# Kernel optimization log

Hardware: AMD Instinct MI355X
Metric: run time of the kernel (lower is better)

The kernel has to match this reference:

```python
import jax, jax.numpy as jnp
import numpy as np

N, C, SI, VI, H, R = 10000, 2, 128, 16, 4, 32
SH, VH = SI // H, VI // H  # 32, 4
EPS = 1e-8

def _vnorm(x, axis):
    # clamped L2 norm, matches _norm_no_nan
    return jnp.sqrt(jnp.clip(jnp.sum(x * x, axis=axis), EPS, None))

def _gvp_full(s, v, wh, ws_w, ws_b, wv, wsv_w, wsv_b):
    # GVP with activations=(silu, sigmoid), vector_gate=True, vi=vo
    vh = jnp.swapaxes(v, -1, -2) @ wh            # [..., 3, h]
    vn = _vnorm(vh, -2)                          # [..., h]
    so = jnp.concatenate([s, vn], -1) @ ws_w + ws_b
    vo = jnp.swapaxes(vh @ wv, -1, -2)           # [..., vo, 3]
    gate = jax.nn.sigmoid(jax.nn.sigmoid(so) @ wsv_w + wsv_b)
    return jax.nn.silu(so), vo * gate[..., None]

def setup_inputs():
    key = jax.random.key(0)
    ks = iter(jax.random.split(key, 40))
    def lin(i, o):
        return jax.random.normal(next(ks), (i, o), jnp.float32) / np.sqrt(i)
    def bias(o):
        return 0.02 * jax.random.normal(next(ks), (o,), jnp.float32)
    inp = {}
    inp['s'] = jax.random.normal(next(ks), (N, C, SI), jnp.float32)
    inp['v'] = jax.random.normal(next(ks), (N, C, VI, 3), jnp.float32)
    # weight_proj: GVP((SI,VI)->(R,0)), no activations; h_dim = max(VI,0) = VI
    inp['wp_wh'] = lin(VI, VI); inp['wp_ws_w'] = lin(VI + SI, R); inp['wp_ws_b'] = bias(R)
    # to_q/k/v: GVP((SI,VI)->(SI,VI)), silu/sigmoid, vector_gate; h_dim = VI
    for p in ('q', 'k', 'vv'):
        inp[p + '_wh'] = lin(VI, VI)
        inp[p + '_ws_w'] = lin(VI + SI, SI); inp[p + '_ws_b'] = bias(SI)
        inp[p + '_wv'] = lin(VI, VI)
        inp[p + '_wsv_w'] = lin(SI, VI); inp[p + '_wsv_b'] = bias(VI)
    # attn_gvp_long: GVP((2*SH, 2*VH) -> (1,0)), no activations; h_dim = 2*VH
    inp['attn_wh'] = lin(2 * VH, 2 * VH)
    inp['attn_ws_w'] = lin(2 * VH + 2 * SH, 1); inp['attn_ws_b'] = bias(1)
    return inp

def reference(s, v, wp_wh, wp_ws_w, wp_ws_b,
              q_wh, q_ws_w, q_ws_b, q_wv, q_wsv_w, q_wsv_b,
              k_wh, k_ws_w, k_ws_b, k_wv, k_wsv_w, k_wsv_b,
              vv_wh, vv_ws_w, vv_ws_b, vv_wv, vv_wsv_w, vv_wsv_b,
              attn_wh, attn_ws_w, attn_ws_b):
    n, c = s.shape[:2]
    # ---- Compress: softmax-pool N -> R anchors ----
    vh = jnp.swapaxes(v, -1, -2) @ wp_wh          # [N,C,3,VI]
    vn = _vnorm(vh, -2)                            # [N,C,VI]
    pw = jnp.concatenate([s, vn], -1) @ wp_ws_w + wp_ws_b  # [N,C,R]
    pw = jax.nn.softmax(pw, axis=0)                # softmax over nodes
    s_g = jnp.einsum('nca,ncs->acs', pw, s)        # [R,C,SI] (includes transpose(0,1))
    v_g = jnp.einsum('nca,ncvd->acvd', pw, v)      # [R,C,VI,3]
    # ---- q from nodes, k/v from anchors ----
    qs, qv = _gvp_full(s, v, q_wh, q_ws_w, q_ws_b, q_wv, q_wsv_w, q_wsv_b)
    ks, kv = _gvp_full(s_g, v_g, k_wh, k_ws_w, k_ws_b, k_wv, k_wsv_w, k_wsv_b)
    vs, vv_ = _gvp_full(s_g, v_g, vv_wh, vv_ws_w, vv_ws_b, vv_wv, vv_wsv_w, vv_wsv_b)
    qs = qs.reshape(n, c, H, SH); qv = qv.reshape(n, c, H, VH, 3)
    ks = ks.reshape(R, c, H, SH); kv = kv.reshape(R, c, H, VH, 3)
    vs = vs.reshape(R, c, H, SH); vv_ = vv_.reshape(R, c, H, VH, 3)
    # ---- attention GVP on cat(q, k): split weights instead of materializing concat ----
    wh_q, wh_k = attn_wh[:VH], attn_wh[VH:]        # wh @ cat(qv,kv) = qv@wh_q + kv@wh_k
    qh = jnp.swapaxes(qv, -1, -2) @ wh_q           # [N,C,H,3,2VH]
    kh = jnp.swapaxes(kv, -1, -2) @ wh_k           # [R,C,H,3,2VH]
    vn2 = _vnorm(qh[:, None] + kh[None], -2)       # [N,R,C,H,2VH]
    ws_q = attn_ws_w[:SH]; ws_k = attn_ws_w[SH:2 * SH]; ws_n = attn_ws_w[2 * SH:]
    e = (qs @ ws_q)[:, None] + (ks @ ws_k)[None] + vn2 @ ws_n + attn_ws_b  # [N,R,C,H,1]
    e = e[..., 0] / np.sqrt(SH)
    alpha = jax.nn.softmax(e, axis=1)              # softmax over anchors (dim=1)
    # ---- Broadcast: weighted sum of anchor values ----
    out_s = jnp.einsum('nrch,rchd->nchd', alpha, vs).reshape(n, c, SI)
    out_v = jnp.einsum('nrch,rchde->nchde', alpha, vv_).reshape(n, c, VI, 3)
    return out_s, out_v
```

## Files before the change

kernel.cpp:

```cpp
#include <hip/hip_runtime.h>
#include <hip/hip_bf16.h>


#define N_  10000
#define C_  2
#define SI_ 128
#define VI_ 16
#define H_  4
#define R_  32
#define SH_ 32
#define VH_ 4
#define NC_ (N_*C_)

typedef const float* __restrict__ fptr;

__device__ __forceinline__ float sigm(float x){ return 1.f/(1.f+__expf(-x)); }

#define OFF_LG  0
#define OFF_EQH 640000
#define OFF_SG  2720000
#define OFF_ST  2731264
#define OFF_TKH 2731392
#define OFF_TEK 2737536
#define OFF_TVS 2737792
#define OFF_TVV 2745984

__global__ __launch_bounds__(256) void kA(
    fptr s, fptr v,
    fptr wp_wh, fptr wp_ws_w, fptr wp_ws_b,
    fptr q_wh, fptr q_ws_w, fptr q_ws_b, fptr q_wv, fptr q_wsv_w, fptr q_wsv_b,
    fptr attn_wh, fptr attn_ws_w,
    float* __restrict__ lg, float* __restrict__ eqh)
{
  __shared__ __align__(16) float ARENA[160*20];
  __shared__ __align__(16) float VVs[16*48];
  __shared__ __align__(16) float VHQ[16*48];
  __shared__ __align__(16) float SO[16*128];
  __shared__ __align__(16) float GATE[16*16];
  __shared__ __align__(16) float QV[16*48];
  float* const XT  = ARENA;
  float* const SIG = ARENA;

  const int tid  = threadIdx.x;
  const int row0 = blockIdx.x * 16;

  for (int idx = tid; idx < 16*128; idx += 256){
    int r = idx >> 7, j = idx & 127;
    XT[j*20 + r] = s[(row0+r)*128 + j];
  }
  for (int idx = tid; idx < 16*48; idx += 256){
    int r = idx / 48, k = idx - r*48;
    VVs[r*48 + k] = v[(row0+r)*48 + k];
  }
  __syncthreads();

  for (int t = tid; t < 512; t += 256){
    int r = t >> 5, ii = t & 31, path = ii >> 4, i = ii & 15;
    fptr wh = path ? wp_wh : q_wh;
    float h0=0.f, h1=0.f, h2=0.f;
    #pragma unroll
    for (int j = 0; j < 16; j++){
      float w = wh[j*16 + i];
      h0 = fmaf(VVs[r*48 + j*3 + 0], w, h0);
      h1 = fmaf(VVs[r*48 + j*3 + 1], w, h1);
      h2 = fmaf(VVs[r*48 + j*3 + 2], w, h2);
    }
    float vn = sqrtf(fmaxf(h0*h0 + h1*h1 + h2*h2, 1e-8f));
    if (!path){
      VHQ[r*48 +  0 + i] = h0;
      VHQ[r*48 + 16 + i] = h1;
      VHQ[r*48 + 32 + i] = h2;
      XT[(128+i)*20 + r] = vn;
    } else {
      XT[(144+i)*20 + r] = vn;
    }
  }
  __syncthreads();

  const int colA = tid & 127, rgA = tid >> 7;
  float acc[8];
  {
    float bqs = q_ws_b[colA];
    #pragma unroll
    for (int k = 0; k < 8; k++) acc[k] = bqs;
    #pragma unroll 4
    for (int j = 0; j < 144; j++){
      float w = q_ws_w[j*128 + colA];
      const float* xp = &XT[j*20 + rgA*8];
      float4 x0 = *(const float4*)xp;
      float4 x1 = *(const float4*)(xp + 4);
      acc[0] = fmaf(x0.x, w, acc[0]); acc[1] = fmaf(x0.y, w, acc[1]);
      acc[2] = fmaf(x0.z, w, acc[2]); acc[3] = fmaf(x0.w, w, acc[3]);
      acc[4] = fmaf(x1.x, w, acc[4]); acc[5] = fmaf(x1.y, w, acc[5]);
      acc[6] = fmaf(x1.z, w, acc[6]); acc[7] = fmaf(x1.w, w, acc[7]);
    }
  }
  {
    const int col = tid & 31, rg = tid >> 5;
    float bp = wp_ws_b[col];
    float a0 = bp, a1 = bp;
    #pragma unroll 4
    for (int j = 0; j < 144; j++){
      int jj = (j < 128) ? j : (j + 16);
      float w = wp_ws_w[j*32 + col];
      const float* xp = &XT[jj*20 + rg*2];
      a0 = fmaf(xp[0], w, a0);
      a1 = fmaf(xp[1], w, a1);
    }
    const int n = (row0 >> 1) + rg;
    lg[(     col)*N_ + n] = a0;
    lg[(32 + col)*N_ + n] = a1;
  }
  __syncthreads();

  #pragma unroll
  for (int k = 0; k < 8; k++){
    float so = acc[k];
    float sg_ = sigm(so);
    SIG[(rgA*8 + k)*128 + colA] = sg_;
    SO [(rgA*8 + k)*128 + colA] = so * sg_;
  }
  __syncthreads();

  {
    const int r = tid >> 4, g = tid & 15;
    float ga = q_wsv_b[g];
    #pragma unroll 8
    for (int o = 0; o < 128; o += 4){
      float4 s4 = *(const float4*)&SIG[r*128 + o];
      ga = fmaf(s4.x, q_wsv_w[(o+0)*16 + g], ga);
      ga = fmaf(s4.y, q_wsv_w[(o+1)*16 + g], ga);
      ga = fmaf(s4.z, q_wsv_w[(o+2)*16 + g], ga);
      ga = fmaf(s4.w, q_wsv_w[(o+3)*16 + g], ga);
    }
    GATE[r*16 + g] = sigm(ga);
  }
  if (tid < 64){
    const int r = tid >> 2, h = tid & 3;
    float e = 0.f;
    #pragma unroll
    for (int t = 0; t < 32; t++)
      e = fmaf(SO[r*128 + h*32 + t], attn_ws_w[t], e);
    eqh[(row0 + r)*104 + h] = e;
  }
  __syncthreads();

  for (int t = tid; t < 16*48; t += 256){
    int r = t / 48, k = t - r*48, i = k / 3, d = k - i*3;
    float a = 0.f;
    #pragma unroll
    for (int j = 0; j < 16; j++)
      a = fmaf(VHQ[r*48 + d*16 + j], q_wv[j*16 + i], a);
    QV[r*48 + k] = a * GATE[r*16 + i];
  }
  __syncthreads();

  for (int t = tid; t < 16*96; t += 256){
    int r = t / 96, k = t - r*96;
    int h = k / 24, rem = k - h*24, d = rem >> 3, ee = rem & 7;
    float a = 0.f;
    #pragma unroll
    for (int i = 0; i < 4; i++)
      a = fmaf(QV[r*48 + (h*4 + i)*3 + d], attn_wh[i*8 + ee], a);
    eqh[(row0 + r)*104 + 8 + k] = a;
  }
}

__global__ __launch_bounds__(256) void kStats(const float* __restrict__ lg,
                                              float* __restrict__ st)
{
  const int q = blockIdx.x;
  const int tid = threadIdx.x;
  const float* col = lg + q*N_;
  __shared__ float red[256];

  float m = -1e30f;
  for (int n = tid; n < N_; n += 256) m = fmaxf(m, col[n]);
  red[tid] = m; __syncthreads();
  for (int s2 = 128; s2 > 0; s2 >>= 1){
    if (tid < s2) red[tid] = fmaxf(red[tid], red[tid + s2]);
    __syncthreads();
  }
  const float mx = red[0];
  __syncthreads();

  float sm = 0.f;
  for (int n = tid; n < N_; n += 256) sm += __expf(col[n] - mx);
  red[tid] = sm; __syncthreads();
  for (int s2 = 128; s2 > 0; s2 >>= 1){
    if (tid < s2) red[tid] += red[tid + s2];
    __syncthreads();
  }
  if (tid == 0){ st[q*2] = mx; st[q*2 + 1] = red[0]; }
}

#define CHUNK_ 50
__global__ __launch_bounds__(256) void kAccum(const float* __restrict__ lg,
                                              const float* __restrict__ st,
                                              fptr s, fptr v,
                                              float* __restrict__ sg)
{
  const int b = blockIdx.x, c = b & 1, chunk = b >> 1;
  const int n0 = chunk * CHUNK_;
  const int tid = threadIdx.x;
  const int ag = tid >> 5, dl = tid & 31;

  float mx[4], dn[4];
  #pragma unroll
  for (int aa = 0; aa < 4; aa++){
    int a = ag*4 + aa;
    mx[aa] = st[(c*32 + a)*2];
    dn[aa] = 1.f / st[(c*32 + a)*2 + 1];
  }
  float acc[4][6] = {};
  for (int n = n0; n < n0 + CHUNK_; n++){
    const int rc = n*2 + c;
    float pw[4];
    #pragma unroll
    for (int aa = 0; aa < 4; aa++)
      pw[aa] = __expf(lg[(c*32 + ag*4 + aa)*N_ + n] - mx[aa]) * dn[aa];
    #pragma unroll
    for (int dd = 0; dd < 6; dd++){
      int d = dl + 32*dd;
      if (d < 176){
        float xv = (d < 128) ? s[rc*128 + d] : v[rc*48 + d - 128];
        #pragma unroll
        for (int aa = 0; aa < 4; aa++)
          acc[aa][dd] = fmaf(pw[aa], xv, acc[aa][dd]);
      }
    }
  }
  #pragma unroll
  for (int aa = 0; aa < 4; aa++)
    #pragma unroll
    for (int dd = 0; dd < 6; dd++){
      int d = dl + 32*dd;
      if (d < 176)
        atomicAdd(&sg[(c*32 + ag*4 + aa)*176 + d], acc[aa][dd]);
    }
}

__global__ __launch_bounds__(256) void kSmall(
    const float* __restrict__ sg,
    fptr k_wh, fptr k_ws_w, fptr k_ws_b, fptr k_wv, fptr k_wsv_w, fptr k_wsv_b,
    fptr vv_wh, fptr vv_ws_w, fptr vv_ws_b, fptr vv_wv, fptr vv_wsv_w, fptr vv_wsv_b,
    fptr attn_wh, fptr attn_ws_w,
    float* __restrict__ tkh, float* __restrict__ tek,
    float* __restrict__ tvs, float* __restrict__ tvv)
{
  const int b = blockIdx.x, r = b >> 1, c = b & 1;
  const int tid = threadIdx.x;
  __shared__ float X[176];
  __shared__ float VN[2][16];
  __shared__ float VH[2][48];
  __shared__ float SOk[128], SOv[128];
  __shared__ float G[2][16];
  __shared__ float KV[48];

  if (tid < 176) X[tid] = sg[(c*32 + r)*176 + tid];
  __syncthreads();

  if (tid < 32){
    int path = tid >> 4, i = tid & 15;
    fptr wh = path ? vv_wh : k_wh;
    float h0=0.f, h1=0.f, h2=0.f;
    #pragma unroll
    for (int j = 0; j < 16; j++){
      float w = wh[j*16 + i];
      h0 = fmaf(X[128 + j*3 + 0], w, h0);
      h1 = fmaf(X[128 + j*3 + 1], w, h1);
      h2 = fmaf(X[128 + j*3 + 2], w, h2);
    }
    VH[path][ 0 + i] = h0; VH[path][16 + i] = h1; VH[path][32 + i] = h2;
    VN[path][i] = sqrtf(fmaxf(h0*h0 + h1*h1 + h2*h2, 1e-8f));
  }
  __syncthreads();

  {
    int path = tid >> 7, col = tid & 127;
    fptr W  = path ? vv_ws_w : k_ws_w;
    fptr Bb = path ? vv_ws_b : k_ws_b;
    float so = Bb[col];
    for (int j = 0; j < 128; j++) so = fmaf(X[j], W[j*128 + col], so);
    #pragma unroll
    for (int i = 0; i < 16; i++)  so = fmaf(VN[path][i], W[(128+i)*128 + col], so);
    (path ? SOv : SOk)[col] = so;
  }
  __syncthreads();

  if (tid < 32){
    int path = tid >> 4, g = tid & 15;
    fptr Wsv = path ? vv_wsv_w : k_wsv_w;
    fptr Bsv = path ? vv_wsv_b : k_wsv_b;
    const float* SOp = path ? SOv : SOk;
    float ga = Bsv[g];
    for (int o = 0; o < 128; o++)
      ga = fmaf(sigm(SOp[o]), Wsv[o*16 + g], ga);
    G[path][g] = sigm(ga);
  } else if (tid < 36){
    int h = tid - 32;
    float e = 0.f;
    #pragma unroll
    for (int t = 0; t < 32; t++){
      float so = SOk[h*32 + t];
      e = fmaf(so * sigm(so), attn_ws_w[32 + t], e);
    }
    tek[(r*2 + c)*4 + h] = e;
  } else if (tid >= 64 && tid < 192){
    int o = tid - 64;
    float so = SOv[o];
    tvs[(r*2 + c)*128 + o] = so * sigm(so);
  }
  __syncthreads();

  if (tid < 96){
    int path = tid / 48, k = tid % 48, i = k / 3, d = k - i*3;
    fptr Wv = path ? vv_wv : k_wv;
    float vo = 0.f;
    #pragma unroll
    for (int j = 0; j < 16; j++)
      vo = fmaf(VH[path][d*16 + j], Wv[j*16 + i], vo);
    float gv = vo * G[path][i];
    if (path == 0) KV[k] = gv;
    else {
      int h = i >> 2, ii = i & 3;
      tvv[(((r*2 + c)*4 + h)*4 + ii)*3 + d] = gv;
    }
  }
  __syncthreads();

  if (tid < 96){
    int h = tid / 24, rem = tid % 24, d = rem >> 3, ee = rem & 7;
    float a = 0.f;
    #pragma unroll
    for (int i = 0; i < 4; i++)
      a = fmaf(KV[(h*4 + i)*3 + d], attn_wh[(4 + i)*8 + ee], a);
    tkh[((r*2 + c)*4 + h)*24 + d*8 + ee] = a;
  }
}

__global__ __launch_bounds__(512) void kAttn(
    const float* __restrict__ eqh,
    const float* __restrict__ tkh, const float* __restrict__ tek,
    const float* __restrict__ tvs, const float* __restrict__ tvv,
    fptr attn_ws_w, fptr attn_ws_b,
    float* __restrict__ out)
{
  __shared__ __align__(16) float KH[6144];
  __shared__ __align__(16) float EK[256];
  __shared__ __align__(16) float VS[256*36];
  __shared__ __align__(16) float VVt[3072];
  const int tid = threadIdx.x;

  for (int i = tid; i < 6144; i += 512) KH[i] = tkh[i];
  if (tid < 256) EK[tid] = tek[tid];
  for (int i = tid; i < 8192; i += 512){ int base = i >> 5, t = i & 31; VS[base*36 + t] = tvs[i]; }
  for (int i = tid; i < 3072; i += 512) VVt[i] = tvv[i];

  float wsn[8];
  #pragma unroll
  for (int ee = 0; ee < 8; ee++) wsn[ee] = attn_ws_w[64 + ee];
  const float wb = attn_ws_b[0];
  __syncthreads();

  const int row = blockIdx.x*128 + (tid >> 2);
  const int h = tid & 3;
  if (row < NC_){
    const int c = row & 1;
    const float eq = eqh[row*104 + h];
    float qh[24];
    const float4* qp = (const float4*)&eqh[row*104 + 8 + h*24];
    #pragma unroll
    for (int k = 0; k < 6; k++){
      float4 t4 = qp[k];
      qh[k*4+0] = t4.x; qh[k*4+1] = t4.y; qh[k*4+2] = t4.z; qh[k*4+3] = t4.w;
    }
    float e[32];
    float em = -1e30f;
    #pragma unroll
    for (int r = 0; r < 32; r++){
      const int base = (r*2 + c)*4 + h;
      const float* khp = &KH[base*24];
      float en = 0.f;
      #pragma unroll
      for (int ee = 0; ee < 8; ee++){
        float a0 = qh[ee]      + khp[ee];
        float a1 = qh[8 + ee]  + khp[8 + ee];
        float a2 = qh[16 + ee] + khp[16 + ee];
        en = fmaf(sqrtf(fmaxf(a0*a0 + a1*a1 + a2*a2, 1e-8f)), wsn[ee], en);
      }
      float ev = (eq + EK[base] + en + wb) * 0.17677669529663687f;
      e[r] = ev; em = fmaxf(em, ev);
    }
    float den = 0.f;
    #pragma unroll
    for (int r = 0; r < 32; r++){ e[r] = __expf(e[r] - em); den += e[r]; }
    const float inv = 1.f / den;
    float accs[32] = {};
    float accv[12] = {};
    #pragma unroll
    for (int r = 0; r < 32; r++){
      const int base = (r*2 + c)*4 + h;
      const float al = e[r] * inv;
      const float* vsp = &VS[base*36];
      #pragma unroll
      for (int t = 0; t < 32; t++) accs[t] = fmaf(al, vsp[t], accs[t]);
      const float* vvp = &VVt[base*12];
      #pragma unroll
      for (int k = 0; k < 12; k++) accv[k] = fmaf(al, vvp[k], accv[k]);
    }
    float* po = &out[row*128 + h*32];
    #pragma unroll
    for (int t = 0; t < 32; t++) po[t] = accs[t];
    float* pv = &out[NC_*128 + row*48 + h*12];
    #pragma unroll
    for (int k = 0; k < 12; k++) pv[k] = accv[k];
  }
}

extern "C" void kernel_launch(void* const* d_in, const int* in_sizes, int n_in,
                              void* d_out, int out_size, void* d_ws, size_t ws_size,
                              hipStream_t stream)
{
  fptr s        = (fptr)d_in[0];
  fptr v        = (fptr)d_in[1];
  fptr wp_wh    = (fptr)d_in[2];
  fptr wp_ws_w  = (fptr)d_in[3];
  fptr wp_ws_b  = (fptr)d_in[4];
  fptr q_wh     = (fptr)d_in[5];
  fptr q_ws_w   = (fptr)d_in[6];
  fptr q_ws_b   = (fptr)d_in[7];
  fptr q_wv     = (fptr)d_in[8];
  fptr q_wsv_w  = (fptr)d_in[9];
  fptr q_wsv_b  = (fptr)d_in[10];
  fptr k_wh     = (fptr)d_in[11];
  fptr k_ws_w   = (fptr)d_in[12];
  fptr k_ws_b   = (fptr)d_in[13];
  fptr k_wv     = (fptr)d_in[14];
  fptr k_wsv_w  = (fptr)d_in[15];
  fptr k_wsv_b  = (fptr)d_in[16];
  fptr vv_wh    = (fptr)d_in[17];
  fptr vv_ws_w  = (fptr)d_in[18];
  fptr vv_ws_b  = (fptr)d_in[19];
  fptr vv_wv    = (fptr)d_in[20];
  fptr vv_wsv_w = (fptr)d_in[21];
  fptr vv_wsv_b = (fptr)d_in[22];
  fptr attn_wh  = (fptr)d_in[23];
  fptr attn_ws_w= (fptr)d_in[24];
  fptr attn_ws_b= (fptr)d_in[25];

  float* ws  = (float*)d_ws;
  float* lg  = ws + OFF_LG;
  float* eqh = ws + OFF_EQH;
  float* sg  = ws + OFF_SG;
  float* st  = ws + OFF_ST;
  float* tkh = ws + OFF_TKH;
  float* tek = ws + OFF_TEK;
  float* tvs = ws + OFF_TVS;
  float* tvv = ws + OFF_TVV;

  hipMemsetAsync(sg, 0, 11264*sizeof(float), stream);

  kA<<<NC_/16, 256, 0, stream>>>(s, v, wp_wh, wp_ws_w, wp_ws_b,
                                 q_wh, q_ws_w, q_ws_b, q_wv, q_wsv_w, q_wsv_b,
                                 attn_wh, attn_ws_w, lg, eqh);
  kStats<<<64, 256, 0, stream>>>(lg, st);
  kAccum<<<2*(N_/CHUNK_), 256, 0, stream>>>(lg, st, s, v, sg);
  kSmall<<<64, 256, 0, stream>>>(sg,
                                 k_wh, k_ws_w, k_ws_b, k_wv, k_wsv_w, k_wsv_b,
                                 vv_wh, vv_ws_w, vv_ws_b, vv_wv, vv_wsv_w, vv_wsv_b,
                                 attn_wh, attn_ws_w, tkh, tek, tvs, tvv);
  kAttn<<<(NC_ + 127)/128, 512, 0, stream>>>(eqh, tkh, tek, tvs, tvv,
                                             attn_ws_w, attn_ws_b, (float*)d_out);
}
```

Before: 253.2 us.

## Enlarge kA row tile, replace atomics with chunk partials, vectorize attention loads

```diff
diff --git a/kernel.cpp b/kernel.cpp
--- a/kernel.cpp
+++ b/kernel.cpp
@@ -16,45 +16,48 @@
 
 __device__ __forceinline__ float sigm(float x){ return 1.f/(1.f+__expf(-x)); }
 
-#define OFF_LG  0
-#define OFF_EQH 640000
-#define OFF_SG  2720000
-#define OFF_ST  2731264
-#define OFF_TKH 2731392
-#define OFF_TEK 2737536
-#define OFF_TVS 2737792
-#define OFF_TVV 2745984
-
-__global__ __launch_bounds__(256) void kA(
+#define OFF_LG   0
+#define OFF_EQH  640000
+#define OFF_ST   2731264
+#define OFF_TKH  2731392
+#define OFF_TEK  2737536
+#define OFF_TVS  2737792
+#define OFF_TVV  2745984
+#define OFF_PART 2749056
+
+#define CHUNK_  200
+#define NCHUNK_ (N_/CHUNK_)
+
+__global__ __launch_bounds__(512) void kA(
     fptr s, fptr v,
     fptr wp_wh, fptr wp_ws_w, fptr wp_ws_b,
     fptr q_wh, fptr q_ws_w, fptr q_ws_b, fptr q_wv, fptr q_wsv_w, fptr q_wsv_b,
     fptr attn_wh, fptr attn_ws_w,
     float* __restrict__ lg, float* __restrict__ eqh)
 {
-  __shared__ __align__(16) float ARENA[160*20];
-  __shared__ __align__(16) float VVs[16*48];
-  __shared__ __align__(16) float VHQ[16*48];
-  __shared__ __align__(16) float SO[16*128];
-  __shared__ __align__(16) float GATE[16*16];
-  __shared__ __align__(16) float QV[16*48];
+  __shared__ __align__(16) float ARENA[160*36];
+  __shared__ __align__(16) float VVs[32*48];
+  __shared__ __align__(16) float VHQ[32*48];
+  __shared__ __align__(16) float SO[32*128];
+  __shared__ __align__(16) float GATE[32*16];
+  __shared__ __align__(16) float QV[32*48];
   float* const XT  = ARENA;
   float* const SIG = ARENA;
 
   const int tid  = threadIdx.x;
-  const int row0 = blockIdx.x * 16;
-
-  for (int idx = tid; idx < 16*128; idx += 256){
+  const int row0 = blockIdx.x * 32;
+
+  for (int idx = tid; idx < 32*128; idx += 512){
     int r = idx >> 7, j = idx & 127;
-    XT[j*20 + r] = s[(row0+r)*128 + j];
-  }
-  for (int idx = tid; idx < 16*48; idx += 256){
+    XT[j*36 + r] = s[(row0+r)*128 + j];
+  }
+  for (int idx = tid; idx < 32*48; idx += 512){
     int r = idx / 48, k = idx - r*48;
     VVs[r*48 + k] = v[(row0+r)*48 + k];
   }
   __syncthreads();
 
-  for (int t = tid; t < 512; t += 256){
+  for (int t = tid; t < 1024; t += 512){
     int r = t >> 5, ii = t & 31, path = ii >> 4, i = ii & 15;
     fptr wh = path ? wp_wh : q_wh;
     float h0=0.f, h1=0.f, h2=0.f;
@@ -70,9 +73,9 @@
       VHQ[r*48 +  0 + i] = h0;
       VHQ[r*48 + 16 + i] = h1;
       VHQ[r*48 + 32 + i] = h2;
-      XT[(128+i)*20 + r] = vn;
+      XT[(128+i)*36 + r] = vn;
     } else {
-      XT[(144+i)*20 + r] = vn;
+      XT[(144+i)*36 + r] = vn;
     }
   }
   __syncthreads();
@@ -86,7 +89,7 @@
     #pragma unroll 4
     for (int j = 0; j < 144; j++){
       float w = q_ws_w[j*128 + colA];
-      const float* xp = &XT[j*20 + rgA*8];
+      const float* xp = &XT[j*36 + rgA*8];
       float4 x0 = *(const float4*)xp;
       float4 x1 = *(const float4*)(xp + 4);
       acc[0] = fmaf(x0.x, w, acc[0]); acc[1] = fmaf(x0.y, w, acc[1]);
@@ -103,7 +106,7 @@
     for (int j = 0; j < 144; j++){
       int jj = (j < 128) ? j : (j + 16);
       float w = wp_ws_w[j*32 + col];
-      const float* xp = &XT[jj*20 + rg*2];
+      const float* xp = &XT[jj*36 + rg*2];
       a0 = fmaf(xp[0], w, a0);
       a1 = fmaf(xp[1], w, a1);
     }
@@ -135,7 +138,7 @@
     }
     GATE[r*16 + g] = sigm(ga);
   }
-  if (tid < 64){
+  if (tid < 128){
     const int r = tid >> 2, h = tid & 3;
     float e = 0.f;
     #pragma unroll
@@ -145,7 +148,7 @@
   }
   __syncthreads();
 
-  for (int t = tid; t < 16*48; t += 256){
+  for (int t = tid; t < 32*48; t += 512){
     int r = t / 48, k = t - r*48, i = k / 3, d = k - i*3;
     float a = 0.f;
     #pragma unroll
@@ -155,7 +158,7 @@
   }
   __syncthreads();
 
-  for (int t = tid; t < 16*96; t += 256){
+  for (int t = tid; t < 32*96; t += 512){
     int r = t / 96, k = t - r*96;
     int h = k / 24, rem = k - h*24, d = rem >> 3, ee = rem & 7;
     float a = 0.f;
@@ -194,11 +197,10 @@
   if (tid == 0){ st[q*2] = mx; st[q*2 + 1] = red[0]; }
 }
 
-#define CHUNK_ 50
 __global__ __launch_bounds__(256) void kAccum(const float* __restrict__ lg,
                                               const float* __restrict__ st,
                                               fptr s, fptr v,
-                                              float* __restrict__ sg)
+                                              float* __restrict__ part)
 {
   const int b = blockIdx.x, c = b & 1, chunk = b >> 1;
   const int n0 = chunk * CHUNK_;
@@ -236,12 +238,12 @@
     for (int dd = 0; dd < 6; dd++){
       int d = dl + 32*dd;
       if (d < 176)
-        atomicAdd(&sg[(c*32 + ag*4 + aa)*176 + d], acc[aa][dd]);
+        part[(chunk*64 + c*32 + ag*4 + aa)*176 + d] = acc[aa][dd];
     }
 }
 
 __global__ __launch_bounds__(256) void kSmall(
-    const float* __restrict__ sg,
+    const float* __restrict__ part,
     fptr k_wh, fptr k_ws_w, fptr k_ws_b, fptr k_wv, fptr k_wsv_w, fptr k_wsv_b,
     fptr vv_wh, fptr vv_ws_w, fptr vv_ws_b, fptr vv_wv, fptr vv_wsv_w, fptr vv_wsv_b,
     fptr attn_wh, fptr attn_ws_w,
@@ -257,7 +259,12 @@
   __shared__ float G[2][16];
   __shared__ float KV[48];
 
-  if (tid < 176) X[tid] = sg[(c*32 + r)*176 + tid];
+  if (tid < 176){
+    float x = 0.f;
+    const float* p = part + (c*32 + r)*176 + tid;
+    for (int ch = 0; ch < NCHUNK_; ch++) x += p[(size_t)ch*64*176];
+    X[tid] = x;
+  }
   __syncthreads();
 
   if (tid < 32){
@@ -380,13 +387,19 @@
     #pragma unroll
     for (int r = 0; r < 32; r++){
       const int base = (r*2 + c)*4 + h;
-      const float* khp = &KH[base*24];
+      float khl[24];
+      const float4* kp4 = (const float4*)&KH[base*24];
+      #pragma unroll
+      for (int q = 0; q < 6; q++){
+        float4 t4 = kp4[q];
+        khl[q*4+0] = t4.x; khl[q*4+1] = t4.y; khl[q*4+2] = t4.z; khl[q*4+3] = t4.w;
+      }
       float en = 0.f;
       #pragma unroll
       for (int ee = 0; ee < 8; ee++){
-        float a0 = qh[ee]      + khp[ee];
-        float a1 = qh[8 + ee]  + khp[8 + ee];
-        float a2 = qh[16 + ee] + khp[16 + ee];
+        float a0 = qh[ee]      + khl[ee];
+        float a1 = qh[8 + ee]  + khl[8 + ee];
+        float a2 = qh[16 + ee] + khl[16 + ee];
         en = fmaf(sqrtf(fmaxf(a0*a0 + a1*a1 + a2*a2, 1e-8f)), wsn[ee], en);
       }
       float ev = (eq + EK[base] + en + wb) * 0.17677669529663687f;
@@ -402,12 +415,24 @@
     for (int r = 0; r < 32; r++){
       const int base = (r*2 + c)*4 + h;
       const float al = e[r] * inv;
-      const float* vsp = &VS[base*36];
+      const float4* vp4 = (const float4*)&VS[base*36];
       #pragma unroll
-      for (int t = 0; t < 32; t++) accs[t] = fmaf(al, vsp[t], accs[t]);
-      const float* vvp = &VVt[base*12];
+      for (int q = 0; q < 8; q++){
+        float4 t4 = vp4[q];
+        accs[q*4+0] = fmaf(al, t4.x, accs[q*4+0]);
+        accs[q*4+1] = fmaf(al, t4.y, accs[q*4+1]);
+        accs[q*4+2] = fmaf(al, t4.z, accs[q*4+2]);
+        accs[q*4+3] = fmaf(al, t4.w, accs[q*4+3]);
+      }
+      const float4* vv4 = (const float4*)&VVt[base*12];
       #pragma unroll
-      for (int k = 0; k < 12; k++) accv[k] = fmaf(al, vvp[k], accv[k]);
+      for (int q = 0; q < 3; q++){
+        float4 t4 = vv4[q];
+        accv[q*4+0] = fmaf(al, t4.x, accv[q*4+0]);
+        accv[q*4+1] = fmaf(al, t4.y, accv[q*4+1]);
+        accv[q*4+2] = fmaf(al, t4.z, accv[q*4+2]);
+        accv[q*4+3] = fmaf(al, t4.w, accv[q*4+3]);
+      }
     }
     float* po = &out[row*128 + h*32];
     #pragma unroll
@@ -449,24 +474,22 @@
   fptr attn_ws_w= (fptr)d_in[24];
   fptr attn_ws_b= (fptr)d_in[25];
 
-  float* ws  = (float*)d_ws;
-  float* lg  = ws + OFF_LG;
-  float* eqh = ws + OFF_EQH;
-  float* sg  = ws + OFF_SG;
-  float* st  = ws + OFF_ST;
-  float* tkh = ws + OFF_TKH;
-  float* tek = ws + OFF_TEK;
-  float* tvs = ws + OFF_TVS;
-  float* tvv = ws + OFF_TVV;
-
-  hipMemsetAsync(sg, 0, 11264*sizeof(float), stream);
-
-  kA<<<NC_/16, 256, 0, stream>>>(s, v, wp_wh, wp_ws_w, wp_ws_b,
+  float* ws   = (float*)d_ws;
+  float* lg   = ws + OFF_LG;
+  float* eqh  = ws + OFF_EQH;
+  float* st   = ws + OFF_ST;
+  float* tkh  = ws + OFF_TKH;
+  float* tek  = ws + OFF_TEK;
+  float* tvs  = ws + OFF_TVS;
+  float* tvv  = ws + OFF_TVV;
+  float* part = ws + OFF_PART;
+
+  kA<<<NC_/32, 512, 0, stream>>>(s, v, wp_wh, wp_ws_w, wp_ws_b,
                                  q_wh, q_ws_w, q_ws_b, q_wv, q_wsv_w, q_wsv_b,
                                  attn_wh, attn_ws_w, lg, eqh);
   kStats<<<64, 256, 0, stream>>>(lg, st);
-  kAccum<<<2*(N_/CHUNK_), 256, 0, stream>>>(lg, st, s, v, sg);
-  kSmall<<<64, 256, 0, stream>>>(sg,
+  kAccum<<<2*NCHUNK_, 256, 0, stream>>>(lg, st, s, v, part);
+  kSmall<<<64, 256, 0, stream>>>(part,
                                  k_wh, k_ws_w, k_ws_b, k_wv, k_wsv_w, k_wsv_b,
                                  vv_wh, vv_ws_w, vv_ws_b, vv_wv, vv_wsv_w, vv_wsv_b,
                                  attn_wh, attn_ws_w, tkh, tek, tvs, tvv);
```

New measurement: 320.5 us. +26.6%, slower.
